# Performance work log

Measured on AMD Instinct MI355X. Metric: run time of the kernel, lower is better.

The kernel has to match this reference:

```python
import jax, jax.numpy as jnp
import numpy as np

N = 100000      # user + item nodes
E = 600000      # number of edges
LATDIM = 128
HEAD = 4
HDIM = LATDIM // HEAD


def setup_inputs() -> dict:
    key = jax.random.key(0)
    ks = jax.random.split(key, 7)
    return {
        "embeds": jax.random.normal(ks[0], (N, LATDIM), dtype=jnp.float32),
        "qTrans": jax.random.normal(ks[1], (LATDIM, LATDIM), dtype=jnp.float32) * (1.0 / np.sqrt(LATDIM)),
        "kTrans": jax.random.normal(ks[2], (LATDIM, LATDIM), dtype=jnp.float32) * (1.0 / np.sqrt(LATDIM)),
        "vTrans": jax.random.normal(ks[3], (LATDIM, LATDIM), dtype=jnp.float32) * (1.0 / np.sqrt(LATDIM)),
        "filt": jax.random.normal(ks[4], (N, HEAD), dtype=jnp.float32),
        "rows": jax.random.randint(ks[5], (E,), 0, N, dtype=jnp.int32),
        "cols": jax.random.randint(ks[6], (E,), 0, N, dtype=jnp.int32),
    }


def reference(embeds, qTrans, kTrans, vTrans, filt, rows, cols):
    # gather endpoint embeddings: [E, latdim]
    rowEmbeds = embeds[rows]
    colEmbeds = embeds[cols]
    # per-edge multi-head q/k/v: [E, H, D]
    qEmbeds = (rowEmbeds @ qTrans).reshape(E, HEAD, HDIM)
    kEmbeds = (colEmbeds @ kTrans).reshape(E, HEAD, HDIM)
    vEmbeds = (colEmbeds @ vTrans).reshape(E, HEAD, HDIM)
    # per-edge per-head attention logits
    att = jnp.einsum('ehd,ehd->eh', qEmbeds, kEmbeds)
    att = jnp.clip(att, -10.0, 10.0)
    att = att + filt[cols]
    expAtt = jnp.exp(att)
    # segment softmax over destination rows
    attNorm = jax.ops.segment_sum(expAtt, rows, num_segments=N)[rows]
    att = expAtt / (attNorm + 1e-8)
    # weighted values, scatter-sum back to nodes
    resEdges = (att[:, :, None] * vEmbeds).reshape(E, LATDIM)
    resEmbeds = jax.ops.segment_sum(resEdges, rows, num_segments=N)
    return resEmbeds
```

## Files before the change

kernel.cpp:

```cpp
#include <hip/hip_runtime.h>

#define N_NODES 100000
#define E_EDGES 600000
#define LATDIM 128
#define HEAD 4
#define HDIM 32

#define SCAN_NB 98

typedef __bf16 bf16x8 __attribute__((ext_vector_type(8)));
typedef float  f32x4  __attribute__((ext_vector_type(4)));

__device__ __forceinline__ unsigned f32_to_bf16_rne(float x) {
    unsigned u = __float_as_uint(x);
    u += 0x7fffu + ((u >> 16) & 1u);
    return u >> 16;
}

__device__ __forceinline__ void bf16_split(float x, unsigned& hi, unsigned& lo) {
    unsigned hb = f32_to_bf16_rne(x);
    float hf = __uint_as_float(hb << 16);
    unsigned lb = f32_to_bf16_rne(x - hf);
    hi = hb; lo = lb;
}

__global__ __launch_bounds__(256) void wprep_kernel(
    const float* __restrict__ qT, const float* __restrict__ kT,
    const float* __restrict__ vT,
    unsigned short* __restrict__ WThi, unsigned short* __restrict__ WTlo,
    int* __restrict__ counts, unsigned* __restrict__ state)
{
    int g = blockIdx.x * 256 + threadIdx.x;

    for (int i = g; i < N_NODES; i += SCAN_NB * 256) counts[i] = 0;
    if (g < 128) state[g] = 0u;

    if (g >= 3072) return;
    int m    = g >> 10;
    int rem  = g & 1023;
    int c    = rem >> 3;
    int k0   = (rem & 7) * 16;
    const float* W = (m == 0) ? qT : (m == 1) ? kT : vT;

    unsigned short hi[16], lo[16];
    #pragma unroll
    for (int j = 0; j < 16; ++j) {
        float x = W[(size_t)(k0 + j) * 128 + c];
        unsigned hb, lb;
        bf16_split(x, hb, lb);
        hi[j] = (unsigned short)hb;
        lo[j] = (unsigned short)lb;
    }
    size_t off = (size_t)m * 16384 + (size_t)c * 128 + k0;
    *(uint4*)(WThi + off)     = *(const uint4*)&hi[0];
    *(uint4*)(WThi + off + 8) = *(const uint4*)&hi[8];
    *(uint4*)(WTlo + off)     = *(const uint4*)&lo[0];
    *(uint4*)(WTlo + off + 8) = *(const uint4*)&lo[8];
}

__global__ __launch_bounds__(512, 2) void qkv_mfma_kernel(
    const float* __restrict__ embeds,
    const unsigned short* __restrict__ WThi,
    const unsigned short* __restrict__ WTlo,
    const int* __restrict__ rows,
    int* __restrict__ counts,
    float* __restrict__ Q, unsigned* __restrict__ KV)
{
    __shared__ __align__(16) char smem[65536];
    char* Ahi = smem;
    char* Alo = smem + 32768;
    char* B0h = smem;
    char* B0l = smem + 16384;
    char* B1h = smem + 32768;
    char* B1l = smem + 49152;

    const int tid = threadIdx.x;
    const int rowBase = blockIdx.x * 128;

    uint4 pbh0, pbh1, pbl0, pbl1;

#define PF(MN, HN) do {                                                          \
        const char* _sh = (const char*)(WThi + (size_t)(MN) * 16384 + (size_t)(HN) * 8192); \
        const char* _sl = (const char*)(WTlo + (size_t)(MN) * 16384 + (size_t)(HN) * 8192); \
        pbh0 = *(const uint4*)(_sh + (size_t)tid * 16);                          \
        pbh1 = *(const uint4*)(_sh + (size_t)(512 + tid) * 16);                  \
        pbl0 = *(const uint4*)(_sl + (size_t)tid * 16);                          \
        pbl1 = *(const uint4*)(_sl + (size_t)(512 + tid) * 16);                  \
    } while (0)

#define COMMIT(BHI, BLO) do {                                                    \
        { int _i = tid; int _c = _i >> 4;                                        \
          int _s = (_c * 256 + (_i & 15) * 16) ^ ((_c & 7) << 4);                \
          *(uint4*)((BHI) + _s) = pbh0; *(uint4*)((BLO) + _s) = pbl0; }          \
        { int _i = 512 + tid; int _c = _i >> 4;                                  \
          int _s = (_c * 256 + (_i & 15) * 16) ^ ((_c & 7) << 4);                \
          *(uint4*)((BHI) + _s) = pbh1; *(uint4*)((BLO) + _s) = pbl1; }          \
    } while (0)

#define MFMA_PANEL(ACC, BHI, BLO) do {                                           \
        _Pragma("unroll")                                                        \
        for (int kk = 0; kk < 4; ++kk) {                                         \
            _Pragma("unroll")                                                    \
            for (int n = 0; n < 4; ++n) {                                        \
                int brow = n * 16 + lrow;                                        \
                int byte = brow * 256 + kk * 64 + kg * 16;                       \
                int swz  = byte ^ ((lrow & 7) << 4);                             \
                bf16x8 bh = __builtin_bit_cast(bf16x8, *(const uint4*)((BHI) + swz)); \
                bf16x8 bl = __builtin_bit_cast(bf16x8, *(const uint4*)((BLO) + swz)); \
                ACC[n] = __builtin_amdgcn_mfma_f32_16x16x32_bf16(a_hi[kk], bh, ACC[n], 0, 0, 0); \
                ACC[n] = __builtin_amdgcn_mfma_f32_16x16x32_bf16(a_lo[kk], bh, ACC[n], 0, 0, 0); \
                ACC[n] = __builtin_amdgcn_mfma_f32_16x16x32_bf16(a_hi[kk], bl, ACC[n], 0, 0, 0); \
            }                                                                    \
        }                                                                        \
    } while (0)

#define ZACC(ACC) f32x4 ACC[4] = { {0.f,0.f,0.f,0.f}, {0.f,0.f,0.f,0.f},         \
                                   {0.f,0.f,0.f,0.f}, {0.f,0.f,0.f,0.f} }

#define STORE_Q(ACC, H) do {                                                     \
        _Pragma("unroll")                                                        \
        for (int n = 0; n < 4; ++n)                                              \
        _Pragma("unroll")                                                        \
        for (int j = 0; j < 4; ++j) {                                            \
            int gr  = rowBase + wv * 16 + orow + j;                              \
            int col = (H) * 64 + n * 16 + lrow;                                  \
            if (gr < N_NODES) Q[(size_t)gr * 128 + col] = ACC[n][j];             \
        }                                                                        \
    } while (0)

#define STORE_KV(ACC, H) do {                                                    \
        _Pragma("unroll")                                                        \
        for (int n = 0; n < 4; ++n)                                              \
        _Pragma("unroll")                                                        \
        for (int j = 0; j < 4; ++j) {                                            \
            int gr  = rowBase + wv * 16 + orow + j;                              \
            int col = (H) * 64 + n * 16 + lrow;                                  \
            if (gr < N_NODES) {                                                  \
                unsigned pk = f32_to_bf16_rne(kreg[n][j])                        \
                            | (f32_to_bf16_rne(ACC[n][j]) << 16);                \
                KV[(size_t)gr * 128 + col] = pk;                                 \
            }                                                                    \
        }                                                                        \
    } while (0)

    PF(0, 0);

    for (int e = blockIdx.x * 512 + tid; e < E_EDGES; e += gridDim.x * 512)
        atomicAdd(&counts[rows[e]], 1);

    #pragma unroll
    for (int it = 0; it < 8; ++it) {
        int idx = it * 512 + tid;
        int r  = idx >> 5;
        int c4 = idx & 31;
        int gr = rowBase + r;
        float4 v = make_float4(0.f, 0.f, 0.f, 0.f);
        if (gr < N_NODES) v = ((const float4*)embeds)[(size_t)gr * 32 + c4];
        unsigned hx, lx, hy, ly, hz, lz, hw, lw;
        bf16_split(v.x, hx, lx); bf16_split(v.y, hy, ly);
        bf16_split(v.z, hz, lz); bf16_split(v.w, hw, lw);
        uint2 hp = make_uint2(hx | (hy << 16), hz | (hw << 16));
        uint2 lp = make_uint2(lx | (ly << 16), lz | (lw << 16));
        int byte = r * 256 + c4 * 8;
        int swz  = byte ^ ((r & 7) << 4);
        *(uint2*)(Ahi + swz) = hp;
        *(uint2*)(Alo + swz) = lp;
    }
    __syncthreads();

    const int lane = tid & 63;
    const int wv   = tid >> 6;
    const int lrow = lane & 15;
    const int kg   = lane >> 4;
    const int arow = wv * 16 + lrow;
    const int orow = kg << 2;

    bf16x8 a_hi[4], a_lo[4];
    #pragma unroll
    for (int kk = 0; kk < 4; ++kk) {
        int byte = arow * 256 + kk * 64 + kg * 16;
        int swz  = byte ^ ((lrow & 7) << 4);
        a_hi[kk] = __builtin_bit_cast(bf16x8, *(const uint4*)(Ahi + swz));
        a_lo[kk] = __builtin_bit_cast(bf16x8, *(const uint4*)(Alo + swz));
    }
    __syncthreads();

    COMMIT(B0h, B0l);
    __syncthreads();

    f32x4 kreg[4];

    {
        PF(1, 0); ZACC(acc);
        MFMA_PANEL(acc, B0h, B0l);
        STORE_Q(acc, 0);
        COMMIT(B1h, B1l); __syncthreads();
    }
    {
        PF(2, 0); ZACC(acc);
        MFMA_PANEL(acc, B1h, B1l);
        kreg[0] = acc[0]; kreg[1] = acc[1]; kreg[2] = acc[2]; kreg[3] = acc[3];
        COMMIT(B0h, B0l); __syncthreads();
    }
    {
        PF(0, 1); ZACC(acc);
        MFMA_PANEL(acc, B0h, B0l);
        STORE_KV(acc, 0);
        COMMIT(B1h, B1l); __syncthreads();
    }
    {
        PF(1, 1); ZACC(acc);
        MFMA_PANEL(acc, B1h, B1l);
        STORE_Q(acc, 1);
        COMMIT(B0h, B0l); __syncthreads();
    }
    {
        PF(2, 1); ZACC(acc);
        MFMA_PANEL(acc, B0h, B0l);
        kreg[0] = acc[0]; kreg[1] = acc[1]; kreg[2] = acc[2]; kreg[3] = acc[3];
        COMMIT(B1h, B1l); __syncthreads();
    }
    {
        ZACC(acc);
        MFMA_PANEL(acc, B1h, B1l);
        STORE_KV(acc, 1);
    }

#undef PF
#undef COMMIT
#undef MFMA_PANEL
#undef ZACC
#undef STORE_Q
#undef STORE_KV
}

__global__ __launch_bounds__(256) void scan_lb_kernel(
    const int* __restrict__ counts, int* __restrict__ starts,
    int* __restrict__ cursor, unsigned* __restrict__ state)
{
    __shared__ int s[256];
    __shared__ int bcast;
    int b = blockIdx.x, t = threadIdx.x;
    int base = b * 1024 + t * 4;
    int v0 = (base + 0 < N_NODES) ? counts[base + 0] : 0;
    int v1 = (base + 1 < N_NODES) ? counts[base + 1] : 0;
    int v2 = (base + 2 < N_NODES) ? counts[base + 2] : 0;
    int v3 = (base + 3 < N_NODES) ? counts[base + 3] : 0;
    int local = v0 + v1 + v2 + v3;
    s[t] = local;
    __syncthreads();
    for (int off = 1; off < 256; off <<= 1) {
        int x = (t >= off) ? s[t - off] : 0;
        __syncthreads();
        s[t] += x;
        __syncthreads();
    }
    int incl  = s[t];
    int excl  = incl - local;
    int total = s[255];

    if (t == 0) {
        int sum = 0;
        if (b == 0) {
            atomicExch(&state[0], ((unsigned)total << 2) | 2u);
        } else {
            atomicExch(&state[b], ((unsigned)total << 2) | 1u);
            int i = b - 1;
            while (true) {
                unsigned w = atomicAdd(&state[i], 0u);
                unsigned st = w & 3u;
                if (st == 0u) continue;
                sum += (int)(w >> 2);
                if (st == 2u) break;
                --i;
            }
            atomicExch(&state[b], ((unsigned)(sum + total) << 2) | 2u);
        }
        bcast = sum;
    }
    __syncthreads();
    int e = excl + bcast;
    if (base + 0 < N_NODES) { starts[base + 0] = e;                cursor[base + 0] = e; }
    if (base + 1 < N_NODES) { starts[base + 1] = e + v0;           cursor[base + 1] = e + v0; }
    if (base + 2 < N_NODES) { starts[base + 2] = e + v0 + v1;      cursor[base + 2] = e + v0 + v1; }
    if (base + 3 < N_NODES) { starts[base + 3] = e + v0 + v1 + v2; cursor[base + 3] = e + v0 + v1 + v2; }
}

__global__ __launch_bounds__(256) void scatter_kernel(
    const int* __restrict__ rows, const int* __restrict__ cols,
    int* __restrict__ cursor, int* __restrict__ csrCols)
{
    int e = blockIdx.x * 256 + threadIdx.x;
    if (e >= E_EDGES) return;
    int pos = atomicAdd(&cursor[rows[e]], 1);
    csrCols[pos] = cols[e];
}

__global__ __launch_bounds__(256) void att_agg_kernel(
    const float* __restrict__ Q, const unsigned* __restrict__ KV,
    const float* __restrict__ filt,
    const int* __restrict__ starts, const int* __restrict__ counts,
    const int* __restrict__ csrCols,
    float* __restrict__ out)
{
    int t = threadIdx.x;
    int node = blockIdx.x * 8 + (t >> 5);
    if (node >= N_NODES) return;
    int lane = t & 31;
    int h = lane >> 3;

    float4 q = ((const float4*)(Q + (size_t)node * 128))[lane];
    int s   = starts[node];
    int cnt = counts[node];

    float norm = 0.f;
    float ax = 0.f, ay = 0.f, az = 0.f, aw = 0.f;

    int i = 0;
    for (; i + 2 <= cnt; i += 2) {
        int c0 = csrCols[s + i];
        int c1 = csrCols[s + i + 1];
        uint4 kv0 = ((const uint4*)KV)[(size_t)c0 * 32 + lane];
        uint4 kv1 = ((const uint4*)KV)[(size_t)c1 * 32 + lane];
        float f0 = filt[c0 * HEAD + h];
        float f1 = filt[c1 * HEAD + h];

        float k0x = __uint_as_float(kv0.x << 16), v0x = __uint_as_float(kv0.x & 0xffff0000u);
        float k0y = __uint_as_float(kv0.y << 16), v0y = __uint_as_float(kv0.y & 0xffff0000u);
        float k0z = __uint_as_float(kv0.z << 16), v0z = __uint_as_float(kv0.z & 0xffff0000u);
        float k0w = __uint_as_float(kv0.w << 16), v0w = __uint_as_float(kv0.w & 0xffff0000u);
        float k1x = __uint_as_float(kv1.x << 16), v1x = __uint_as_float(kv1.x & 0xffff0000u);
        float k1y = __uint_as_float(kv1.y << 16), v1y = __uint_as_float(kv1.y & 0xffff0000u);
        float k1z = __uint_as_float(kv1.z << 16), v1z = __uint_as_float(kv1.z & 0xffff0000u);
        float k1w = __uint_as_float(kv1.w << 16), v1w = __uint_as_float(kv1.w & 0xffff0000u);

        float p0 = q.x * k0x + q.y * k0y + q.z * k0z + q.w * k0w;
        float p1 = q.x * k1x + q.y * k1y + q.z * k1z + q.w * k1w;
        p0 += __shfl_xor(p0, 1);   p1 += __shfl_xor(p1, 1);
        p0 += __shfl_xor(p0, 2);   p1 += __shfl_xor(p1, 2);
        p0 += __shfl_xor(p0, 4);   p1 += __shfl_xor(p1, 4);

        float w0 = __expf(fminf(fmaxf(p0, -10.f), 10.f) + f0);
        float w1 = __expf(fminf(fmaxf(p1, -10.f), 10.f) + f1);
        norm += w0 + w1;
        ax += w0 * v0x + w1 * v1x;
        ay += w0 * v0y + w1 * v1y;
        az += w0 * v0z + w1 * v1z;
        aw += w0 * v0w + w1 * v1w;
    }
    if (i < cnt) {
        int c0 = csrCols[s + i];
        uint4 kv0 = ((const uint4*)KV)[(size_t)c0 * 32 + lane];
        float f0 = filt[c0 * HEAD + h];
        float k0x = __uint_as_float(kv0.x << 16), v0x = __uint_as_float(kv0.x & 0xffff0000u);
        float k0y = __uint_as_float(kv0.y << 16), v0y = __uint_as_float(kv0.y & 0xffff0000u);
        float k0z = __uint_as_float(kv0.z << 16), v0z = __uint_as_float(kv0.z & 0xffff0000u);
        float k0w = __uint_as_float(kv0.w << 16), v0w = __uint_as_float(kv0.w & 0xffff0000u);
        float p0 = q.x * k0x + q.y * k0y + q.z * k0z + q.w * k0w;
        p0 += __shfl_xor(p0, 1);
        p0 += __shfl_xor(p0, 2);
        p0 += __shfl_xor(p0, 4);
        float w0 = __expf(fminf(fmaxf(p0, -10.f), 10.f) + f0);
        norm += w0;
        ax += w0 * v0x; ay += w0 * v0y; az += w0 * v0z; aw += w0 * v0w;
    }
    float inv = 1.0f / (norm + 1e-8f);
    ((float4*)(out + (size_t)node * 128))[lane] =
        make_float4(ax * inv, ay * inv, az * inv, aw * inv);
}

extern "C" void kernel_launch(void* const* d_in, const int* in_sizes, int n_in,
                              void* d_out, int out_size, void* d_ws, size_t ws_size,
                              hipStream_t stream) {
    const float* embeds = (const float*)d_in[0];
    const float* qT     = (const float*)d_in[1];
    const float* kT     = (const float*)d_in[2];
    const float* vT     = (const float*)d_in[3];
    const float* filt   = (const float*)d_in[4];
    const int*   rows   = (const int*)d_in[5];
    const int*   cols   = (const int*)d_in[6];
    float*       out    = (float*)d_out;

    float*    Q  = (float*)d_ws;
    unsigned* KV = (unsigned*)(Q + (size_t)N_NODES * 128);
    int* counts    = (int*)(KV + (size_t)N_NODES * 128);
    int* starts    = counts + N_NODES;
    int* cursor    = starts + N_NODES;
    int* csrCols   = cursor + N_NODES;
    unsigned* state = (unsigned*)(csrCols + E_EDGES);

    unsigned short* WThi = (unsigned short*)csrCols;
    unsigned short* WTlo = WThi + 3 * 128 * 128;

    wprep_kernel<<<SCAN_NB, 256, 0, stream>>>(qT, kT, vT, WThi, WTlo, counts, state);
    qkv_mfma_kernel<<<(N_NODES + 127) / 128, 512, 0, stream>>>(
        embeds, WThi, WTlo, rows, counts, Q, KV);
    scan_lb_kernel<<<SCAN_NB, 256, 0, stream>>>(counts, starts, cursor, state);
    scatter_kernel<<<(E_EDGES + 255) / 256, 256, 0, stream>>>(rows, cols, cursor, csrCols);
    att_agg_kernel<<<(N_NODES + 7) / 8, 256, 0, stream>>>(
        Q, KV, filt, starts, counts, csrCols, out);
}
```

Before: 272.4 us.

## Switch QKV projection to single-pass fp16 MFMA with persistent weight tiles

Replaces the three-pass bf16 hi/lo split-precision projection with a single fp16 MFMA pass. Embeddings are converted to fp16 in registers straight from global memory rather than staged through shared memory. Each block now keeps one half of all three weight matrices resident in shared memory and loops over 256 rows, which drops the per-panel weight double-buffering and most of the barriers. The risk is lower precision: fp16 has fewer mantissa bits than the split scheme, and large values could overflow or lose accuracy.

```diff
diff --git a/kernel.cpp b/kernel.cpp
--- a/kernel.cpp
+++ b/kernel.cpp
@@ -7,9 +7,11 @@
 #define HDIM 32
 
 #define SCAN_NB 98
-
-typedef __bf16 bf16x8 __attribute__((ext_vector_type(8)));
-typedef float  f32x4  __attribute__((ext_vector_type(4)));
+#define NCHUNK 391
+#define QKV_GRID (NCHUNK * 2)
+
+typedef _Float16 f16x8 __attribute__((ext_vector_type(8)));
+typedef float    f32x4 __attribute__((ext_vector_type(4)));
 
 __device__ __forceinline__ unsigned f32_to_bf16_rne(float x) {
     unsigned u = __float_as_uint(x);
@@ -17,17 +19,10 @@
     return u >> 16;
 }
 
-__device__ __forceinline__ void bf16_split(float x, unsigned& hi, unsigned& lo) {
-    unsigned hb = f32_to_bf16_rne(x);
-    float hf = __uint_as_float(hb << 16);
-    unsigned lb = f32_to_bf16_rne(x - hf);
-    hi = hb; lo = lb;
-}
-
 __global__ __launch_bounds__(256) void wprep_kernel(
     const float* __restrict__ qT, const float* __restrict__ kT,
     const float* __restrict__ vT,
-    unsigned short* __restrict__ WThi, unsigned short* __restrict__ WTlo,
+    unsigned short* __restrict__ WT,
     int* __restrict__ counts, unsigned* __restrict__ state)
 {
     int g = blockIdx.x * 256 + threadIdx.x;
@@ -42,196 +37,123 @@
     int k0   = (rem & 7) * 16;
     const float* W = (m == 0) ? qT : (m == 1) ? kT : vT;
 
-    unsigned short hi[16], lo[16];
+    unsigned short hv[16];
     #pragma unroll
     for (int j = 0; j < 16; ++j) {
-        float x = W[(size_t)(k0 + j) * 128 + c];
-        unsigned hb, lb;
-        bf16_split(x, hb, lb);
-        hi[j] = (unsigned short)hb;
-        lo[j] = (unsigned short)lb;
+        _Float16 h = (_Float16)W[(size_t)(k0 + j) * 128 + c];
+        hv[j] = __builtin_bit_cast(unsigned short, h);
     }
     size_t off = (size_t)m * 16384 + (size_t)c * 128 + k0;
-    *(uint4*)(WThi + off)     = *(const uint4*)&hi[0];
-    *(uint4*)(WThi + off + 8) = *(const uint4*)&hi[8];
-    *(uint4*)(WTlo + off)     = *(const uint4*)&lo[0];
-    *(uint4*)(WTlo + off + 8) = *(const uint4*)&lo[8];
-}
-
-__global__ __launch_bounds__(512, 2) void qkv_mfma_kernel(
+    *(uint4*)(WT + off)     = *(const uint4*)&hv[0];
+    *(uint4*)(WT + off + 8) = *(const uint4*)&hv[8];
+}
+
+__global__ __launch_bounds__(256) void qkv_mfma_kernel(
     const float* __restrict__ embeds,
-    const unsigned short* __restrict__ WThi,
-    const unsigned short* __restrict__ WTlo,
+    const unsigned short* __restrict__ WT,
     const int* __restrict__ rows,
     int* __restrict__ counts,
     float* __restrict__ Q, unsigned* __restrict__ KV)
 {
-    __shared__ __align__(16) char smem[65536];
-    char* Ahi = smem;
-    char* Alo = smem + 32768;
-    char* B0h = smem;
-    char* B0l = smem + 16384;
-    char* B1h = smem + 32768;
-    char* B1l = smem + 49152;
-
-    const int tid = threadIdx.x;
-    const int rowBase = blockIdx.x * 128;
-
-    uint4 pbh0, pbh1, pbl0, pbl1;
-
-#define PF(MN, HN) do {                                                          \
-        const char* _sh = (const char*)(WThi + (size_t)(MN) * 16384 + (size_t)(HN) * 8192); \
-        const char* _sl = (const char*)(WTlo + (size_t)(MN) * 16384 + (size_t)(HN) * 8192); \
-        pbh0 = *(const uint4*)(_sh + (size_t)tid * 16);                          \
-        pbh1 = *(const uint4*)(_sh + (size_t)(512 + tid) * 16);                  \
-        pbl0 = *(const uint4*)(_sl + (size_t)tid * 16);                          \
-        pbl1 = *(const uint4*)(_sl + (size_t)(512 + tid) * 16);                  \
-    } while (0)
-
-#define COMMIT(BHI, BLO) do {                                                    \
-        { int _i = tid; int _c = _i >> 4;                                        \
-          int _s = (_c * 256 + (_i & 15) * 16) ^ ((_c & 7) << 4);                \
-          *(uint4*)((BHI) + _s) = pbh0; *(uint4*)((BLO) + _s) = pbl0; }          \
-        { int _i = 512 + tid; int _c = _i >> 4;                                  \
-          int _s = (_c * 256 + (_i & 15) * 16) ^ ((_c & 7) << 4);                \
-          *(uint4*)((BHI) + _s) = pbh1; *(uint4*)((BLO) + _s) = pbl1; }          \
-    } while (0)
-
-#define MFMA_PANEL(ACC, BHI, BLO) do {                                           \
+    __shared__ __align__(16) char smem[49152];
+
+    const int tid  = threadIdx.x;
+    const int half = blockIdx.x & 1;
+    const int chunk = blockIdx.x >> 1;
+
+    #pragma unroll
+    for (int it = 0; it < 12; ++it) {
+        const int m   = it >> 2;
+        const int idx = (it & 3) * 256 + tid;
+        uint4 v = *(const uint4*)((const char*)(WT + (size_t)m * 16384
+                                                   + (size_t)half * 8192) + idx * 16);
+        int c = idx >> 4;
+        int b = (c * 256 + (idx & 15) * 16) ^ ((c & 7) << 4);
+        *(uint4*)(smem + m * 16384 + b) = v;
+    }
+    __syncthreads();
+
+    const int lane = tid & 63;
+    const int wv   = tid >> 6;
+    const int lrow = lane & 15;
+    const int kg   = lane >> 4;
+
+    for (int t = 0; t < 4; ++t) {
+        const int rowT = chunk * 256 + t * 64 + wv * 16;
+        const int arow = rowT + lrow;
+        const bool rok = arow < N_NODES;
+
+        f16x8 a[4];
+        #pragma unroll
+        for (int kk = 0; kk < 4; ++kk) {
+            float4 u0 = make_float4(0.f, 0.f, 0.f, 0.f), u1 = u0;
+            if (rok) {
+                const float* p = embeds + (size_t)arow * 128 + kk * 32 + kg * 8;
+                u0 = *(const float4*)p;
+                u1 = *(const float4*)(p + 4);
+            }
+            a[kk][0] = (_Float16)u0.x; a[kk][1] = (_Float16)u0.y;
+            a[kk][2] = (_Float16)u0.z; a[kk][3] = (_Float16)u0.w;
+            a[kk][4] = (_Float16)u1.x; a[kk][5] = (_Float16)u1.y;
+            a[kk][6] = (_Float16)u1.z; a[kk][7] = (_Float16)u1.w;
+        }
+
+#define MFMA_M(ACC, M) do {                                                      \
         _Pragma("unroll")                                                        \
         for (int kk = 0; kk < 4; ++kk) {                                         \
             _Pragma("unroll")                                                    \
             for (int n = 0; n < 4; ++n) {                                        \
-                int brow = n * 16 + lrow;                                        \
-                int byte = brow * 256 + kk * 64 + kg * 16;                       \
-                int swz  = byte ^ ((lrow & 7) << 4);                             \
-                bf16x8 bh = __builtin_bit_cast(bf16x8, *(const uint4*)((BHI) + swz)); \
-                bf16x8 bl = __builtin_bit_cast(bf16x8, *(const uint4*)((BLO) + swz)); \
-                ACC[n] = __builtin_amdgcn_mfma_f32_16x16x32_bf16(a_hi[kk], bh, ACC[n], 0, 0, 0); \
-                ACC[n] = __builtin_amdgcn_mfma_f32_16x16x32_bf16(a_lo[kk], bh, ACC[n], 0, 0, 0); \
-                ACC[n] = __builtin_amdgcn_mfma_f32_16x16x32_bf16(a_hi[kk], bl, ACC[n], 0, 0, 0); \
+                int col  = n * 16 + lrow;                                        \
+                int byte = (col * 256 + kk * 64 + kg * 16) ^ ((lrow & 7) << 4);  \
+                f16x8 b = __builtin_bit_cast(f16x8,                              \
+                          *(const uint4*)(smem + (M) * 16384 + byte));           \
+                ACC[n] = __builtin_amdgcn_mfma_f32_16x16x32_f16(a[kk], b, ACC[n], 0, 0, 0); \
             }                                                                    \
         }                                                                        \
     } while (0)
 
-#define ZACC(ACC) f32x4 ACC[4] = { {0.f,0.f,0.f,0.f}, {0.f,0.f,0.f,0.f},         \
-                                   {0.f,0.f,0.f,0.f}, {0.f,0.f,0.f,0.f} }
-
-#define STORE_Q(ACC, H) do {                                                     \
-        _Pragma("unroll")                                                        \
-        for (int n = 0; n < 4; ++n)                                              \
-        _Pragma("unroll")                                                        \
-        for (int j = 0; j < 4; ++j) {                                            \
-            int gr  = rowBase + wv * 16 + orow + j;                              \
-            int col = (H) * 64 + n * 16 + lrow;                                  \
-            if (gr < N_NODES) Q[(size_t)gr * 128 + col] = ACC[n][j];             \
-        }                                                                        \
-    } while (0)
-
-#define STORE_KV(ACC, H) do {                                                    \
-        _Pragma("unroll")                                                        \
-        for (int n = 0; n < 4; ++n)                                              \
-        _Pragma("unroll")                                                        \
-        for (int j = 0; j < 4; ++j) {                                            \
-            int gr  = rowBase + wv * 16 + orow + j;                              \
-            int col = (H) * 64 + n * 16 + lrow;                                  \
-            if (gr < N_NODES) {                                                  \
-                unsigned pk = f32_to_bf16_rne(kreg[n][j])                        \
-                            | (f32_to_bf16_rne(ACC[n][j]) << 16);                \
-                KV[(size_t)gr * 128 + col] = pk;                                 \
-            }                                                                    \
-        }                                                                        \
-    } while (0)
-
-    PF(0, 0);
-
-    for (int e = blockIdx.x * 512 + tid; e < E_EDGES; e += gridDim.x * 512)
+        f32x4 kreg[4];
+        {
+            f32x4 acc[4] = { {0.f,0.f,0.f,0.f}, {0.f,0.f,0.f,0.f},
+                             {0.f,0.f,0.f,0.f}, {0.f,0.f,0.f,0.f} };
+            MFMA_M(acc, 0);
+            #pragma unroll
+            for (int n = 0; n < 4; ++n)
+                #pragma unroll
+                for (int j = 0; j < 4; ++j) {
+                    int gr  = rowT + kg * 4 + j;
+                    int col = half * 64 + n * 16 + lrow;
+                    if (gr < N_NODES) Q[(size_t)gr * 128 + col] = acc[n][j];
+                }
+        }
+        {
+            f32x4 acc[4] = { {0.f,0.f,0.f,0.f}, {0.f,0.f,0.f,0.f},
+                             {0.f,0.f,0.f,0.f}, {0.f,0.f,0.f,0.f} };
+            MFMA_M(acc, 1);
+            kreg[0] = acc[0]; kreg[1] = acc[1]; kreg[2] = acc[2]; kreg[3] = acc[3];
+        }
+        {
+            f32x4 acc[4] = { {0.f,0.f,0.f,0.f}, {0.f,0.f,0.f,0.f},
+                             {0.f,0.f,0.f,0.f}, {0.f,0.f,0.f,0.f} };
+            MFMA_M(acc, 2);
+            #pragma unroll
+            for (int n = 0; n < 4; ++n)
+                #pragma unroll
+                for (int j = 0; j < 4; ++j) {
+                    int gr  = rowT + kg * 4 + j;
+                    int col = half * 64 + n * 16 + lrow;
+                    if (gr < N_NODES) {
+                        unsigned pk = f32_to_bf16_rne(kreg[n][j])
+                                    | (f32_to_bf16_rne(acc[n][j]) << 16);
+                        KV[(size_t)gr * 128 + col] = pk;
+                    }
+                }
+        }
+#undef MFMA_M
+    }
+
+    for (int e = blockIdx.x * 256 + tid; e < E_EDGES; e += QKV_GRID * 256)
         atomicAdd(&counts[rows[e]], 1);
-
-    #pragma unroll
-    for (int it = 0; it < 8; ++it) {
-        int idx = it * 512 + tid;
-        int r  = idx >> 5;
-        int c4 = idx & 31;
-        int gr = rowBase + r;
-        float4 v = make_float4(0.f, 0.f, 0.f, 0.f);
-        if (gr < N_NODES) v = ((const float4*)embeds)[(size_t)gr * 32 + c4];
-        unsigned hx, lx, hy, ly, hz, lz, hw, lw;
-        bf16_split(v.x, hx, lx); bf16_split(v.y, hy, ly);
-        bf16_split(v.z, hz, lz); bf16_split(v.w, hw, lw);
-        uint2 hp = make_uint2(hx | (hy << 16), hz | (hw << 16));
-        uint2 lp = make_uint2(lx | (ly << 16), lz | (lw << 16));
-        int byte = r * 256 + c4 * 8;
-        int swz  = byte ^ ((r & 7) << 4);
-        *(uint2*)(Ahi + swz) = hp;
-        *(uint2*)(Alo + swz) = lp;
-    }
-    __syncthreads();
-
-    const int lane = tid & 63;
-    const int wv   = tid >> 6;
-    const int lrow = lane & 15;
-    const int kg   = lane >> 4;
-    const int arow = wv * 16 + lrow;
-    const int orow = kg << 2;
-
-    bf16x8 a_hi[4], a_lo[4];
-    #pragma unroll
-    for (int kk = 0; kk < 4; ++kk) {
-        int byte = arow * 256 + kk * 64 + kg * 16;
-        int swz  = byte ^ ((lrow & 7) << 4);
-        a_hi[kk] = __builtin_bit_cast(bf16x8, *(const uint4*)(Ahi + swz));
-        a_lo[kk] = __builtin_bit_cast(bf16x8, *(const uint4*)(Alo + swz));
-    }
-    __syncthreads();
-
-    COMMIT(B0h, B0l);
-    __syncthreads();
-
-    f32x4 kreg[4];
-
-    {
-        PF(1, 0); ZACC(acc);
-        MFMA_PANEL(acc, B0h, B0l);
-        STORE_Q(acc, 0);
-        COMMIT(B1h, B1l); __syncthreads();
-    }
-    {
-        PF(2, 0); ZACC(acc);
-        MFMA_PANEL(acc, B1h, B1l);
-        kreg[0] = acc[0]; kreg[1] = acc[1]; kreg[2] = acc[2]; kreg[3] = acc[3];
-        COMMIT(B0h, B0l); __syncthreads();
-    }
-    {
-        PF(0, 1); ZACC(acc);
-        MFMA_PANEL(acc, B0h, B0l);
-        STORE_KV(acc, 0);
-        COMMIT(B1h, B1l); __syncthreads();
-    }
-    {
-        PF(1, 1); ZACC(acc);
-        MFMA_PANEL(acc, B1h, B1l);
-        STORE_Q(acc, 1);
-        COMMIT(B0h, B0l); __syncthreads();
-    }
-    {
-        PF(2, 1); ZACC(acc);
-        MFMA_PANEL(acc, B0h, B0l);
-        kreg[0] = acc[0]; kreg[1] = acc[1]; kreg[2] = acc[2]; kreg[3] = acc[3];
-        COMMIT(B1h, B1l); __syncthreads();
-    }
-    {
-        ZACC(acc);
-        MFMA_PANEL(acc, B1h, B1l);
-        STORE_KV(acc, 1);
-    }
-
-#undef PF
-#undef COMMIT
-#undef MFMA_PANEL
-#undef ZACC
-#undef STORE_Q
-#undef STORE_KV
 }
 
 __global__ __launch_bounds__(256) void scan_lb_kernel(
@@ -389,12 +311,11 @@
     int* csrCols   = cursor + N_NODES;
     unsigned* state = (unsigned*)(csrCols + E_EDGES);
 
-    unsigned short* WThi = (unsigned short*)csrCols;
-    unsigned short* WTlo = WThi + 3 * 128 * 128;
-
-    wprep_kernel<<<SCAN_NB, 256, 0, stream>>>(qT, kT, vT, WThi, WTlo, counts, state);
-    qkv_mfma_kernel<<<(N_NODES + 127) / 128, 512, 0, stream>>>(
-        embeds, WThi, WTlo, rows, counts, Q, KV);
+    unsigned short* WT = (unsigned short*)csrCols;
+
+    wprep_kernel<<<SCAN_NB, 256, 0, stream>>>(qT, kT, vT, WT, counts, state);
+    qkv_mfma_kernel<<<QKV_GRID, 256, 0, stream>>>(
+        embeds, WT, rows, counts, Q, KV);
     scan_lb_kernel<<<SCAN_NB, 256, 0, stream>>>(counts, starts, cursor, state);
     scatter_kernel<<<(E_EDGES + 255) / 256, 256, 0, stream>>>(rows, cols, cursor, csrCols);
     att_agg_kernel<<<(N_NODES + 7) / 8, 256, 0, stream>>>(
```

Measured after the change: 285.5 us. 4.8% more time.
